# Kernel optimization log

Measured on AMD Instinct MI355X. Metric: run time of the kernel, lower is better.

Reference implementation:

```python
import jax, jax.numpy as jnp
import numpy as np
from jax import lax

# ---- fake-quant helpers (brevitas-style, STE round) ----

def ste_round(x):
    return x + lax.stop_gradient(jnp.round(x) - x)

def qsym(x, bits):
    """Symmetric per-tensor quant with dynamic max-abs scale."""
    qmax = float(2 ** (bits - 1) - 1)
    scale = jnp.max(jnp.abs(x)) / qmax + 1e-8
    return ste_round(jnp.clip(x / scale, -qmax - 1.0, qmax)) * scale

def qfixed(x, scale, lo, hi):
    """Fixed-scale quant (used for bounded activations sigmoid/tanh)."""
    return ste_round(jnp.clip(x / scale, lo, hi)) * scale

def qrelu(x, bits):
    """Unsigned quantized ReLU with dynamic per-tensor scale."""
    qmax = float(2 ** bits - 1)
    r = jax.nn.relu(x)
    scale = jnp.max(r) / qmax + 1e-8
    return ste_round(jnp.clip(r / scale, 0.0, qmax)) * scale

SIG_SCALE = 1.0 / 63.0    # 6-bit unsigned for sigmoid in [0,1]
TANH_SCALE = 1.0 / 31.0   # 6-bit signed for tanh in [-1,1]

IN, H = 10, 20


def setup_inputs() -> dict:
    key = jax.random.key(0)
    ks = jax.random.split(key, 12)
    s = lambda n: 1.0 / np.sqrt(n)
    return {
        "x": jax.random.normal(ks[0], (8192, 256, IN), jnp.float32),
        "w_ih": jax.random.uniform(ks[1], (4 * H, IN), jnp.float32, -s(H), s(H)),
        "w_hh": jax.random.uniform(ks[2], (4 * H, H), jnp.float32, -s(H), s(H)),
        "b_ih": jax.random.uniform(ks[3], (4 * H,), jnp.float32, -s(H), s(H)),
        "b_hh": jax.random.uniform(ks[4], (4 * H,), jnp.float32, -s(H), s(H)),
        "w1": jax.random.uniform(ks[5], (64, H), jnp.float32, -s(H), s(H)),
        "b1": jax.random.uniform(ks[6], (64,), jnp.float32, -s(H), s(H)),
        "w2": jax.random.uniform(ks[7], (32, 64), jnp.float32, -s(64), s(64)),
        "b2": jax.random.uniform(ks[8], (32,), jnp.float32, -s(64), s(64)),
        "w3": jax.random.uniform(ks[9], (5, 32), jnp.float32, -s(32), s(32)),
        "b3": jax.random.uniform(ks[10], (5,), jnp.float32, -s(32), s(32)),
    }


def reference(x, w_ih, w_hh, b_ih, b_hh, w1, b1, w2, b2, w3, b3):
    B, T, _ = x.shape
    # io quant (Int8 per-tensor) on input, 8-bit weight quant
    xq = qsym(x, 8)
    wih_q, whh_q = qsym(w_ih, 8), qsym(w_hh, 8)
    w1q, w2q, w3q = qsym(w1, 8), qsym(w2, 8), qsym(w3, 8)

    # precompute input contribution to gates: [B,T,4H]
    x_gates = jnp.einsum('bti,gi->btg', xq, wih_q) + b_ih + b_hh

    h0 = jnp.zeros((B, H), x.dtype)
    c0 = jnp.zeros((B, H), x.dtype)

    def step(carry, xg):
        h, c = carry
        gates = qsym(xg + h @ whh_q.T, 6)          # 6-bit gate accumulator
        i, f, g, o = jnp.split(gates, 4, axis=-1)   # torch gate order i,f,g,o
        i = qfixed(jax.nn.sigmoid(i), SIG_SCALE, 0.0, 63.0)
        f = qfixed(jax.nn.sigmoid(f), SIG_SCALE, 0.0, 63.0)
        g = qfixed(jnp.tanh(g), TANH_SCALE, -32.0, 31.0)
        o = qfixed(jax.nn.sigmoid(o), SIG_SCALE, 0.0, 63.0)
        c_new = qsym(f * c + i * g, 6)              # 6-bit cell state quant
        h_new = qsym(o * qfixed(jnp.tanh(c_new), TANH_SCALE, -32.0, 31.0), 8)  # io quant
        return (h_new, c_new), None

    (hT, _), _ = lax.scan(step, (h0, c0), jnp.swapaxes(x_gates, 0, 1))

    # dropout is identity in eval mode
    out = qrelu(hT, 6)
    out = qrelu(out @ w1q.T + b1, 6)
    out = qrelu(out @ w2q.T + b2, 6)
    return out @ w3q.T + b3
```

## Files before the change

### kernel.cpp

```cpp
#include <hip/hip_runtime.h>

constexpr int Tn  = 256;
constexpr int INn = 10;
constexpr int Hn  = 20;
constexpr int G4  = 80;
constexpr int Bn  = 8192;

constexpr int NB  = 256;
constexpr int NT  = 256;
constexpr int NW  = NT / 64;
constexpr int BPB = Bn / NB;
constexpr int PREP = 81;

constexpr int RING_U64  = 2 * NB;

constexpr int WS_XMAX   = 1040;
constexpr int WS_SX     = 1041;
constexpr int WS_WIH    = 1088;
constexpr int WS_WHH    = WS_WIH + G4 * INn;
constexpr int WS_W1     = WS_WHH + G4 * Hn;
constexpr int WS_W2     = WS_W1 + 64 * Hn;
constexpr int WS_W3     = WS_W2 + 32 * 64;
constexpr int WS_END    = WS_W3 + 5 * 32;

constexpr float SIGS = (float)(1.0 / 63.0);
constexpr float TANS = (float)(1.0 / 31.0);
constexpr double RS_SIG = 1.0 / (double)SIGS;
constexpr double RS_TAN = 1.0 / (double)TANS;

__device__ __forceinline__ float wave_bmax64(float v) {
#pragma unroll
  for (int off = 32; off; off >>= 1) v = fmaxf(v, __shfl_xor(v, off, 64));
  return v;
}

__device__ __forceinline__ float divrs(float v, double rs) {
  return (float)((double)v * rs);
}
__device__ __forceinline__ float quantq(float v, float s, float lo, float hi) {
  return __fmul_rn(rintf(fminf(fmaxf(v / s, lo), hi)), s);
}
__device__ __forceinline__ float quantr(float v, double rs, float s, float lo,
                                        float hi) {
  return __fmul_rn(rintf(fminf(fmaxf(divrs(v, rs), lo), hi)), s);
}
__device__ __forceinline__ float sigm(float v) {
  return 1.0f / (1.0f + expf(-v));
}

__device__ __forceinline__ unsigned long long ring_ld(unsigned long long* p) {
  return __hip_atomic_load(p, __ATOMIC_RELAXED, __HIP_MEMORY_SCOPE_AGENT);
}
__device__ __forceinline__ void ring_st(unsigned long long* p,
                                        unsigned long long v) {
  __hip_atomic_store(p, v, __ATOMIC_RELAXED, __HIP_MEMORY_SCOPE_AGENT);
}

__device__ __forceinline__ void gm_begin(float v, int inst,
                                         unsigned long long* ring,
                                         float* s_red) {
  const int tid = threadIdx.x;
  v = wave_bmax64(v);
  if ((tid & 63) == 0) s_red[tid >> 6] = v;
  __syncthreads();
  if (tid == 0) {
    float bm = fmaxf(fmaxf(s_red[0], s_red[1]), fmaxf(s_red[2], s_red[3]));
    ring_st(&ring[(inst & 1) * NB + blockIdx.x],
            ((unsigned long long)(unsigned)inst << 32) | __float_as_uint(bm));
  }
}

__device__ __forceinline__ float gm_end(int inst, unsigned long long* ring,
                                        float* s_bc) {
  const int tid = threadIdx.x;
  const unsigned long long tag = (unsigned long long)(unsigned)inst << 32;
  const int base = (inst & 1) * NB;
  if (tid < 64) {
    const int i0 = base + tid * 4;
    unsigned long long w0, w1, w2, w3;
    do {
      w0 = ring_ld(&ring[i0 + 0]);
      w1 = ring_ld(&ring[i0 + 1]);
      w2 = ring_ld(&ring[i0 + 2]);
      w3 = ring_ld(&ring[i0 + 3]);
    } while ((((w0 ^ tag) | (w1 ^ tag) | (w2 ^ tag) | (w3 ^ tag)) >> 32) != 0ull);
    float m = fmaxf(
        fmaxf(__uint_as_float((unsigned)w0), __uint_as_float((unsigned)w1)),
        fmaxf(__uint_as_float((unsigned)w2), __uint_as_float((unsigned)w3)));
    m = wave_bmax64(m);
    if (tid == 0) *s_bc = m;
  }
  __syncthreads();
  return *s_bc;
}

__global__ void k_init(unsigned long long* ring, unsigned* wsu) {
  int i = threadIdx.x;
  if (i < RING_U64) ring[i] = 0xFFFFFFFF00000000ull;
  if (i == 0) wsu[WS_XMAX] = 0u;
}

__global__ void k_xmax(const float4* __restrict__ x4, unsigned* wsu) {
  float m = 0.f;
  int idx = blockIdx.x * blockDim.x + threadIdx.x;
  int stride = gridDim.x * blockDim.x;
  for (int i = idx; i < (Bn * Tn * INn) / 4; i += stride) {
    float4 v = x4[i];
    m = fmaxf(m, fmaxf(fmaxf(fabsf(v.x), fabsf(v.y)),
                       fmaxf(fabsf(v.z), fabsf(v.w))));
  }
  m = wave_bmax64(m);
  __shared__ float sred[4];
  if ((threadIdx.x & 63) == 0) sred[threadIdx.x >> 6] = m;
  __syncthreads();
  if (threadIdx.x == 0) {
    m = fmaxf(fmaxf(sred[0], sred[1]), fmaxf(sred[2], sred[3]));
    atomicMax(&wsu[WS_XMAX], __float_as_uint(m));
  }
}

__device__ void quant_tensor(const float* __restrict__ src, int n, float* dst,
                             float* sred, float* sb, int nt) {
  const int tid = threadIdx.x;
  float m = 0.f;
  for (int i = tid; i < n; i += nt) m = fmaxf(m, fabsf(src[i]));
  m = wave_bmax64(m);
  __syncthreads();
  if ((tid & 63) == 0) sred[tid >> 6] = m;
  __syncthreads();
  if (tid == 0) {
    float bm = sred[0];
    for (int w = 1; w < nt / 64; ++w) bm = fmaxf(bm, sred[w]);
    *sb = __fadd_rn(bm / 127.0f, 1e-8f);
  }
  __syncthreads();
  float s = *sb;
  for (int i = tid; i < n; i += nt) {
    float q = rintf(fminf(fmaxf(src[i] / s, -128.f), 127.f));
    dst[i] = __fmul_rn(q, s);
  }
}

__global__ __launch_bounds__(1024) void k_wq(const float* wih, const float* whh,
                                             const float* w1, const float* w2,
                                             const float* w3, unsigned* wsu) {
  float* wsf = (float*)wsu;
  __shared__ float sred[16];
  __shared__ float sb;
  if (threadIdx.x == 0)
    wsf[WS_SX] = __fadd_rn(__uint_as_float(wsu[WS_XMAX]) / 127.0f, 1e-8f);
  quant_tensor(wih, G4 * INn, wsf + WS_WIH, sred, &sb, 1024);
  quant_tensor(whh, G4 * Hn,  wsf + WS_WHH, sred, &sb, 1024);
  quant_tensor(w1,  64 * Hn,  wsf + WS_W1,  sred, &sb, 1024);
  quant_tensor(w2,  32 * 64,  wsf + WS_W2,  sred, &sb, 1024);
  quant_tensor(w3,  5 * 32,   wsf + WS_W3,  sred, &sb, 1024);
}

__global__ __launch_bounds__(NT, 1) void k_lstm(
    const float* __restrict__ x,
    const float* __restrict__ bih, const float* __restrict__ bhh,
    const float* __restrict__ b1, const float* __restrict__ b2,
    const float* __restrict__ b3,
    float* __restrict__ out, unsigned* __restrict__ wsu) {
  const float* wsf = (const float*)wsu;
  unsigned long long* ring = (unsigned long long*)wsu;

  __shared__ float s_wih[G4][INn];
  __shared__ float s_whh[G4][Hn];
  __shared__ float s_bih[G4], s_bhh[G4];
  __shared__ float s_h[BPB][Hn];
  __shared__ float s_c[BPB][Hn];
  __shared__ float s_pre[BPB][PREP];
  __shared__ float s_xs[BPB][INn];
  __shared__ float s_l2[BPB][32];
  __shared__ float s_red[NW];
  __shared__ float s_bc;

  const int tid = threadIdx.x;
  const int b0 = blockIdx.x * BPB;

  for (int i = tid; i < G4 * INn; i += NT) (&s_wih[0][0])[i] = wsf[WS_WIH + i];
  for (int i = tid; i < G4 * Hn; i += NT) (&s_whh[0][0])[i] = wsf[WS_WHH + i];
  if (tid < G4) { s_bih[tid] = bih[tid]; s_bhh[tid] = bhh[tid]; }
  for (int i = tid; i < BPB * Hn; i += NT) {
    (&s_h[0][0])[i] = 0.f;
    (&s_c[0][0])[i] = 0.f;
  }
  const float sx = wsf[WS_SX];
  const double rsx = 1.0 / (double)sx;

  const int bl = tid >> 3;
  const int g0 = (tid & 7) * 10;

  const int bi0 = tid / INn, ii0 = tid - bi0 * INn;
  const int e1 = NT + tid;
  const int bi1 = e1 / INn, ii1 = e1 - bi1 * INn;
  const bool has1 = (e1 < BPB * INn);

  {
    float v = x[((b0 + bi0) * Tn + 0) * INn + ii0];
    s_xs[bi0][ii0] = __fmul_rn(rintf(fminf(fmaxf(divrs(v, rsx), -128.f), 127.f)), sx);
    if (has1) {
      float v1 = x[((b0 + bi1) * Tn + 0) * INn + ii1];
      s_xs[bi1][ii1] = __fmul_rn(rintf(fminf(fmaxf(divrs(v1, rsx), -128.f), 127.f)), sx);
    }
  }
  __syncthreads();

  float xacc[10];
  {
    float xr[INn];
#pragma unroll
    for (int i = 0; i < INn; i++) xr[i] = s_xs[bl][i];
#pragma unroll
    for (int gg = 0; gg < 10; ++gg) {
      int g = g0 + gg;
      float acc = 0.f;
#pragma unroll
      for (int i = 0; i < INn; i++) acc = fmaf(xr[i], s_wih[g][i], acc);
      acc = __fadd_rn(acc, s_bih[g]);
      xacc[gg] = __fadd_rn(acc, s_bhh[g]);
    }
  }

  int inst = 0;

  for (int t = 0; t < Tn; ++t) {
    const bool more = (t + 1 < Tn);

    float hreg[Hn];
#pragma unroll
    for (int k = 0; k < Hn; k++) hreg[k] = s_h[bl][k];
    float lm = 0.f;
#pragma unroll
    for (int gg = 0; gg < 10; ++gg) {
      int g = g0 + gg;
      float hd = 0.f;
#pragma unroll
      for (int k = 0; k < Hn; k++) hd = fmaf(hreg[k], s_whh[g][k], hd);
      float pre = __fadd_rn(xacc[gg], hd);
      s_pre[bl][g] = pre;
      lm = fmaxf(lm, fabsf(pre));
    }
    gm_begin(lm, inst, ring, s_red);
    float xr0 = 0.f, xr1 = 0.f;
    if (more) {
      xr0 = x[((b0 + bi0) * Tn + (t + 1)) * INn + ii0];
      if (has1) xr1 = x[((b0 + bi1) * Tn + (t + 1)) * INn + ii1];
    }
    float s1v = __fadd_rn(gm_end(inst, ring, &s_bc) / 31.0f, 1e-8f);
    inst++;
    const double rs1 = 1.0 / (double)s1v;

    float cpre[3], og[3], hpre[3];
    float lm2 = 0.f;
#pragma unroll
    for (int k = 0; k < 3; k++) {
      int e = tid + k * NT;
      if (e < BPB * Hn) {
        int cb = e / Hn, j = e - cb * Hn;
        float gi = quantr(s_pre[cb][j],      rs1, s1v, -32.f, 31.f);
        float gf = quantr(s_pre[cb][20 + j], rs1, s1v, -32.f, 31.f);
        float gg = quantr(s_pre[cb][40 + j], rs1, s1v, -32.f, 31.f);
        float go = quantr(s_pre[cb][60 + j], rs1, s1v, -32.f, 31.f);
        float iv = quantr(sigm(gi), RS_SIG, SIGS, 0.f, 63.f);
        float fv = quantr(sigm(gf), RS_SIG, SIGS, 0.f, 63.f);
        float gv = quantr(tanhf(gg), RS_TAN, TANS, -32.f, 31.f);
        og[k]    = quantr(sigm(go), RS_SIG, SIGS, 0.f, 63.f);
        float cp = __fadd_rn(__fmul_rn(fv, s_c[cb][j]), __fmul_rn(iv, gv));
        cpre[k] = cp;
        lm2 = fmaxf(lm2, fabsf(cp));
      }
    }
    gm_begin(lm2, inst, ring, s_red);
    if (more) {
      s_xs[bi0][ii0] = __fmul_rn(rintf(fminf(fmaxf(divrs(xr0, rsx), -128.f), 127.f)), sx);
      if (has1)
        s_xs[bi1][ii1] = __fmul_rn(rintf(fminf(fmaxf(divrs(xr1, rsx), -128.f), 127.f)), sx);
    }
    float s2v = __fadd_rn(gm_end(inst, ring, &s_bc) / 31.0f, 1e-8f);
    inst++;

    float lm3 = 0.f;
#pragma unroll
    for (int k = 0; k < 3; k++) {
      int e = tid + k * NT;
      if (e < BPB * Hn) {
        int cb = e / Hn, j = e - cb * Hn;
        float cn = quantq(cpre[k], s2v, -32.f, 31.f);
        s_c[cb][j] = cn;
        float tq = quantr(tanhf(cn), RS_TAN, TANS, -32.f, 31.f);
        float hp = __fmul_rn(og[k], tq);
        hpre[k] = hp;
        lm3 = fmaxf(lm3, fabsf(hp));
      }
    }
    gm_begin(lm3, inst, ring, s_red);
    if (more) {
      float xr[INn];
#pragma unroll
      for (int i = 0; i < INn; i++) xr[i] = s_xs[bl][i];
#pragma unroll
      for (int gg = 0; gg < 10; ++gg) {
        int g = g0 + gg;
        float acc = 0.f;
#pragma unroll
        for (int i = 0; i < INn; i++) acc = fmaf(xr[i], s_wih[g][i], acc);
        acc = __fadd_rn(acc, s_bih[g]);
        xacc[gg] = __fadd_rn(acc, s_bhh[g]);
      }
    }
    float s3v = __fadd_rn(gm_end(inst, ring, &s_bc) / 127.0f, 1e-8f);
    inst++;

#pragma unroll
    for (int k = 0; k < 3; k++) {
      int e = tid + k * NT;
      if (e < BPB * Hn) {
        int cb = e / Hn, j = e - cb * Hn;
        s_h[cb][j] = quantq(hpre[k], s3v, -128.f, 127.f);
      }
    }
    __syncthreads();
  }

  {
    float r[3];
    float lm = 0.f;
#pragma unroll
    for (int k = 0; k < 3; k++) {
      int e = tid + k * NT;
      if (e < BPB * Hn) {
        r[k] = fmaxf((&s_h[0][0])[e], 0.f);
        lm = fmaxf(lm, r[k]);
      }
    }
    gm_begin(lm, inst, ring, s_red);
    float s = __fadd_rn(gm_end(inst, ring, &s_bc) / 63.0f, 1e-8f);
    inst++;
#pragma unroll
    for (int k = 0; k < 3; k++) {
      int e = tid + k * NT;
      if (e < BPB * Hn)
        (&s_h[0][0])[e] = __fmul_rn(rintf(fminf(fmaxf(r[k] / s, 0.f), 63.f)), s);
    }
  }
  __syncthreads();

  float* s_l1 = &s_pre[0][0];
  {
    float a[8];
    float lm = 0.f;
#pragma unroll
    for (int k = 0; k < 8; k++) {
      int o = tid + k * NT;
      int cb = o >> 6, j = o & 63;
      float acc = 0.f;
#pragma unroll
      for (int kk = 0; kk < Hn; kk++)
        acc = fmaf(s_h[cb][kk], wsf[WS_W1 + j * Hn + kk], acc);
      acc = __fadd_rn(acc, b1[j]);
      acc = fmaxf(acc, 0.f);
      a[k] = acc;
      lm = fmaxf(lm, acc);
    }
    gm_begin(lm, inst, ring, s_red);
    float s = __fadd_rn(gm_end(inst, ring, &s_bc) / 63.0f, 1e-8f);
    inst++;
#pragma unroll
    for (int k = 0; k < 8; k++) {
      int o = tid + k * NT;
      s_l1[o] = __fmul_rn(rintf(fminf(fmaxf(a[k] / s, 0.f), 63.f)), s);
    }
  }
  __syncthreads();

  {
    float a[4];
    float lm = 0.f;
#pragma unroll
    for (int k = 0; k < 4; k++) {
      int o = tid + k * NT;
      int cb = o >> 5, j = o & 31;
      float acc = 0.f;
#pragma unroll
      for (int kk = 0; kk < 64; kk++)
        acc = fmaf(s_l1[cb * 64 + kk], wsf[WS_W2 + j * 64 + kk], acc);
      acc = __fadd_rn(acc, b2[j]);
      acc = fmaxf(acc, 0.f);
      a[k] = acc;
      lm = fmaxf(lm, acc);
    }
    gm_begin(lm, inst, ring, s_red);
    float s = __fadd_rn(gm_end(inst, ring, &s_bc) / 63.0f, 1e-8f);
    inst++;
#pragma unroll
    for (int k = 0; k < 4; k++) {
      int o = tid + k * NT;
      int cb = o >> 5, j = o & 31;
      s_l2[cb][j] = __fmul_rn(rintf(fminf(fmaxf(a[k] / s, 0.f), 63.f)), s);
    }
  }
  __syncthreads();

  if (tid < BPB * 5) {
    int cb = tid / 5, j = tid - cb * 5;
    float acc = 0.f;
#pragma unroll
    for (int kk = 0; kk < 32; kk++)
      acc = fmaf(s_l2[cb][kk], wsf[WS_W3 + j * 32 + kk], acc);
    acc = __fadd_rn(acc, b3[j]);
    out[(b0 + cb) * 5 + j] = acc;
  }
}

extern "C" void kernel_launch(void* const* d_in, const int* in_sizes, int n_in,
                              void* d_out, int out_size, void* d_ws,
                              size_t ws_size, hipStream_t stream) {
  const float* x   = (const float*)d_in[0];
  const float* wih = (const float*)d_in[1];
  const float* whh = (const float*)d_in[2];
  const float* bih = (const float*)d_in[3];
  const float* bhh = (const float*)d_in[4];
  const float* w1  = (const float*)d_in[5];
  const float* b1  = (const float*)d_in[6];
  const float* w2  = (const float*)d_in[7];
  const float* b2  = (const float*)d_in[8];
  const float* w3  = (const float*)d_in[9];
  const float* b3  = (const float*)d_in[10];
  float* out = (float*)d_out;
  unsigned* wsu = (unsigned*)d_ws;
  unsigned long long* ring = (unsigned long long*)d_ws;

  k_init<<<dim3(1), dim3(1024), 0, stream>>>(ring, wsu);
  k_xmax<<<dim3(512), dim3(256), 0, stream>>>((const float4*)x, wsu);
  k_wq<<<dim3(1), dim3(1024), 0, stream>>>(wih, whh, w1, w2, w3, wsu);

  void* args[] = {(void*)&x,  (void*)&bih, (void*)&bhh, (void*)&b1,
                  (void*)&b2, (void*)&b3,  (void*)&out, (void*)&wsu};
  hipLaunchCooperativeKernel(k_lstm, dim3(NB), dim3(NT), args, 0, stream);
}
```

Baseline: 2.048 ms.

## Use fewer, larger blocks to shrink the grid-wide max barrier ring

Cuts the persistent grid from 256 blocks of 256 threads to 64 blocks of 1024 threads. Each grid-wide max-reduction barrier then polls only 64 ring slots, one per lane, instead of four per lane. The block-level reduction now covers a variable number of waves through shuffles, and the spin loop is software-pipelined with two outstanding loads. Each block now holds more batch rows and uses fewer CUs, which risks lower occupancy and lower per-step throughput.

```diff
diff --git a/kernel.cpp b/kernel.cpp
--- a/kernel.cpp
+++ b/kernel.cpp
@@ -6,8 +6,8 @@
 constexpr int G4  = 80;
 constexpr int Bn  = 8192;
 
-constexpr int NB  = 256;
-constexpr int NT  = 256;
+constexpr int NB  = 64;
+constexpr int NT  = 1024;
 constexpr int NW  = NT / 64;
 constexpr int BPB = Bn / NB;
 constexpr int PREP = 81;
@@ -63,31 +63,31 @@
   v = wave_bmax64(v);
   if ((tid & 63) == 0) s_red[tid >> 6] = v;
   __syncthreads();
-  if (tid == 0) {
-    float bm = fmaxf(fmaxf(s_red[0], s_red[1]), fmaxf(s_red[2], s_red[3]));
-    ring_st(&ring[(inst & 1) * NB + blockIdx.x],
-            ((unsigned long long)(unsigned)inst << 32) | __float_as_uint(bm));
+  if (tid < 64) {
+    float bm = (tid < NW) ? s_red[tid] : 0.f;
+#pragma unroll
+    for (int off = 1; off < NW; off <<= 1) bm = fmaxf(bm, __shfl_xor(bm, off, 64));
+    if (tid == 0)
+      ring_st(&ring[(inst & 1) * NB + 0 + blockIdx.x],
+              ((unsigned long long)(unsigned)inst << 32) | __float_as_uint(bm));
   }
 }
 
 __device__ __forceinline__ float gm_end(int inst, unsigned long long* ring,
                                         float* s_bc) {
   const int tid = threadIdx.x;
-  const unsigned long long tag = (unsigned long long)(unsigned)inst << 32;
-  const int base = (inst & 1) * NB;
+  const unsigned ep = (unsigned)inst;
   if (tid < 64) {
-    const int i0 = base + tid * 4;
-    unsigned long long w0, w1, w2, w3;
-    do {
-      w0 = ring_ld(&ring[i0 + 0]);
-      w1 = ring_ld(&ring[i0 + 1]);
-      w2 = ring_ld(&ring[i0 + 2]);
-      w3 = ring_ld(&ring[i0 + 3]);
-    } while ((((w0 ^ tag) | (w1 ^ tag) | (w2 ^ tag) | (w3 ^ tag)) >> 32) != 0ull);
-    float m = fmaxf(
-        fmaxf(__uint_as_float((unsigned)w0), __uint_as_float((unsigned)w1)),
-        fmaxf(__uint_as_float((unsigned)w2), __uint_as_float((unsigned)w3)));
-    m = wave_bmax64(m);
+    unsigned long long* p = &ring[(inst & 1) * NB + tid];
+    unsigned long long cur = ring_ld(p);
+    for (;;) {
+      unsigned long long n1 = ring_ld(p);
+      if (__all((unsigned)(cur >> 32) == ep)) break;
+      unsigned long long n2 = ring_ld(p);
+      if (__all((unsigned)(n1 >> 32) == ep)) { cur = n1; break; }
+      cur = n2;
+    }
+    float m = wave_bmax64(__uint_as_float((unsigned)cur));
     if (tid == 0) *s_bc = m;
   }
   __syncthreads();
```

Result: slower. 3.338 ms (+63.0%).

## Halve grid to 128 blocks with 64 batch rows per block

Applied to the files above, without the earlier changes.

Reduces the persistent grid from 256 to 128 blocks, so each block handles 64 batch rows and each thread computes 20 gates instead of 10. The goal is to cut the cost of the cross-block max-reduction barriers (three per timestep), since each gm_end poll now reads fewer ring slots and fewer blocks must arrive. In exchange, per-block work per step doubles and only half the CUs are used, so the serial per-step compute gets longer.

```diff
diff --git a/kernel.cpp b/kernel.cpp
--- a/kernel.cpp
+++ b/kernel.cpp
@@ -6,10 +6,11 @@
 constexpr int G4  = 80;
 constexpr int Bn  = 8192;
 
-constexpr int NB  = 256;
+constexpr int NB  = 128;
 constexpr int NT  = 256;
 constexpr int NW  = NT / 64;
 constexpr int BPB = Bn / NB;
+constexpr int NGT = 20;
 constexpr int PREP = 81;
 
 constexpr int RING_U64  = 2 * NB;
@@ -76,17 +77,13 @@
   const unsigned long long tag = (unsigned long long)(unsigned)inst << 32;
   const int base = (inst & 1) * NB;
   if (tid < 64) {
-    const int i0 = base + tid * 4;
-    unsigned long long w0, w1, w2, w3;
+    const int i0 = base + tid * 2;
+    unsigned long long w0, w1;
     do {
       w0 = ring_ld(&ring[i0 + 0]);
       w1 = ring_ld(&ring[i0 + 1]);
-      w2 = ring_ld(&ring[i0 + 2]);
-      w3 = ring_ld(&ring[i0 + 3]);
-    } while ((((w0 ^ tag) | (w1 ^ tag) | (w2 ^ tag) | (w3 ^ tag)) >> 32) != 0ull);
-    float m = fmaxf(
-        fmaxf(__uint_as_float((unsigned)w0), __uint_as_float((unsigned)w1)),
-        fmaxf(__uint_as_float((unsigned)w2), __uint_as_float((unsigned)w3)));
+    } while ((((w0 ^ tag) | (w1 ^ tag)) >> 32) != 0ull);
+    float m = fmaxf(__uint_as_float((unsigned)w0), __uint_as_float((unsigned)w1));
     m = wave_bmax64(m);
     if (tid == 0) *s_bc = m;
   }
@@ -189,31 +186,35 @@
   const float sx = wsf[WS_SX];
   const double rsx = 1.0 / (double)sx;
 
-  const int bl = tid >> 3;
-  const int g0 = (tid & 7) * 10;
+  const int bl = tid >> 2;
+  const int g0 = (tid & 3) * NGT;
 
   const int bi0 = tid / INn, ii0 = tid - bi0 * INn;
   const int e1 = NT + tid;
   const int bi1 = e1 / INn, ii1 = e1 - bi1 * INn;
-  const bool has1 = (e1 < BPB * INn);
+  const int e2 = 2 * NT + tid;
+  const int bi2 = e2 / INn, ii2 = e2 - bi2 * INn;
+  const bool has2 = (e2 < BPB * INn);
 
   {
     float v = x[((b0 + bi0) * Tn + 0) * INn + ii0];
     s_xs[bi0][ii0] = __fmul_rn(rintf(fminf(fmaxf(divrs(v, rsx), -128.f), 127.f)), sx);
-    if (has1) {
-      float v1 = x[((b0 + bi1) * Tn + 0) * INn + ii1];
-      s_xs[bi1][ii1] = __fmul_rn(rintf(fminf(fmaxf(divrs(v1, rsx), -128.f), 127.f)), sx);
-    }
-  }
-  __syncthreads();
-
-  float xacc[10];
+    float v1 = x[((b0 + bi1) * Tn + 0) * INn + ii1];
+    s_xs[bi1][ii1] = __fmul_rn(rintf(fminf(fmaxf(divrs(v1, rsx), -128.f), 127.f)), sx);
+    if (has2) {
+      float v2 = x[((b0 + bi2) * Tn + 0) * INn + ii2];
+      s_xs[bi2][ii2] = __fmul_rn(rintf(fminf(fmaxf(divrs(v2, rsx), -128.f), 127.f)), sx);
+    }
+  }
+  __syncthreads();
+
+  float xacc[NGT];
   {
     float xr[INn];
 #pragma unroll
     for (int i = 0; i < INn; i++) xr[i] = s_xs[bl][i];
 #pragma unroll
-    for (int gg = 0; gg < 10; ++gg) {
+    for (int gg = 0; gg < NGT; ++gg) {
       int g = g0 + gg;
       float acc = 0.f;
 #pragma unroll
@@ -233,7 +234,7 @@
     for (int k = 0; k < Hn; k++) hreg[k] = s_h[bl][k];
     float lm = 0.f;
 #pragma unroll
-    for (int gg = 0; gg < 10; ++gg) {
+    for (int gg = 0; gg < NGT; ++gg) {
       int g = g0 + gg;
       float hd = 0.f;
 #pragma unroll
@@ -243,57 +244,56 @@
       lm = fmaxf(lm, fabsf(pre));
     }
     gm_begin(lm, inst, ring, s_red);
-    float xr0 = 0.f, xr1 = 0.f;
+    float xr0 = 0.f, xr1 = 0.f, xr2 = 0.f;
     if (more) {
       xr0 = x[((b0 + bi0) * Tn + (t + 1)) * INn + ii0];
-      if (has1) xr1 = x[((b0 + bi1) * Tn + (t + 1)) * INn + ii1];
+      xr1 = x[((b0 + bi1) * Tn + (t + 1)) * INn + ii1];
+      if (has2) xr2 = x[((b0 + bi2) * Tn + (t + 1)) * INn + ii2];
     }
     float s1v = __fadd_rn(gm_end(inst, ring, &s_bc) / 31.0f, 1e-8f);
     inst++;
     const double rs1 = 1.0 / (double)s1v;
 
-    float cpre[3], og[3], hpre[3];
+    float cpre[5], og[5];
     float lm2 = 0.f;
 #pragma unroll
-    for (int k = 0; k < 3; k++) {
+    for (int k = 0; k < 5; k++) {
       int e = tid + k * NT;
-      if (e < BPB * Hn) {
-        int cb = e / Hn, j = e - cb * Hn;
-        float gi = quantr(s_pre[cb][j],      rs1, s1v, -32.f, 31.f);
-        float gf = quantr(s_pre[cb][20 + j], rs1, s1v, -32.f, 31.f);
-        float gg = quantr(s_pre[cb][40 + j], rs1, s1v, -32.f, 31.f);
-        float go = quantr(s_pre[cb][60 + j], rs1, s1v, -32.f, 31.f);
-        float iv = quantr(sigm(gi), RS_SIG, SIGS, 0.f, 63.f);
-        float fv = quantr(sigm(gf), RS_SIG, SIGS, 0.f, 63.f);
-        float gv = quantr(tanhf(gg), RS_TAN, TANS, -32.f, 31.f);
-        og[k]    = quantr(sigm(go), RS_SIG, SIGS, 0.f, 63.f);
-        float cp = __fadd_rn(__fmul_rn(fv, s_c[cb][j]), __fmul_rn(iv, gv));
-        cpre[k] = cp;
-        lm2 = fmaxf(lm2, fabsf(cp));
-      }
+      int cb = e / Hn, j = e - cb * Hn;
+      float gi = quantr(s_pre[cb][j],      rs1, s1v, -32.f, 31.f);
+      float gf = quantr(s_pre[cb][20 + j], rs1, s1v, -32.f, 31.f);
+      float gg = quantr(s_pre[cb][40 + j], rs1, s1v, -32.f, 31.f);
+      float go = quantr(s_pre[cb][60 + j], rs1, s1v, -32.f, 31.f);
+      float iv = quantr(sigm(gi), RS_SIG, SIGS, 0.f, 63.f);
+      float fv = quantr(sigm(gf), RS_SIG, SIGS, 0.f, 63.f);
+      float gv = quantr(tanhf(gg), RS_TAN, TANS, -32.f, 31.f);
+      og[k]    = quantr(sigm(go), RS_SIG, SIGS, 0.f, 63.f);
+      float cp = __fadd_rn(__fmul_rn(fv, s_c[cb][j]), __fmul_rn(iv, gv));
+      cpre[k] = cp;
+      lm2 = fmaxf(lm2, fabsf(cp));
     }
     gm_begin(lm2, inst, ring, s_red);
     if (more) {
       s_xs[bi0][ii0] = __fmul_rn(rintf(fminf(fmaxf(divrs(xr0, rsx), -128.f), 127.f)), sx);
-      if (has1)
-        s_xs[bi1][ii1] = __fmul_rn(rintf(fminf(fmaxf(divrs(xr1, rsx), -128.f), 127.f)), sx);
+      s_xs[bi1][ii1] = __fmul_rn(rintf(fminf(fmaxf(divrs(xr1, rsx), -128.f), 127.f)), sx);
+      if (has2)
+        s_xs[bi2][ii2] = __fmul_rn(rintf(fminf(fmaxf(divrs(xr2, rsx), -128.f), 127.f)), sx);
     }
     float s2v = __fadd_rn(gm_end(inst, ring, &s_bc) / 31.0f, 1e-8f);
     inst++;
 
+    float hpre[5];
     float lm3 = 0.f;
 #pragma unroll
-    for (int k = 0; k < 3; k++) {
+    for (int k = 0; k < 5; k++) {
       int e = tid + k * NT;
-      if (e < BPB * Hn) {
-        int cb = e / Hn, j = e - cb * Hn;
-        float cn = quantq(cpre[k], s2v, -32.f, 31.f);
-        s_c[cb][j] = cn;
-        float tq = quantr(tanhf(cn), RS_TAN, TANS, -32.f, 31.f);
-        float hp = __fmul_rn(og[k], tq);
-        hpre[k] = hp;
-        lm3 = fmaxf(lm3, fabsf(hp));
-      }
+      int cb = e / Hn, j = e - cb * Hn;
+      float cn = quantq(cpre[k], s2v, -32.f, 31.f);
+      s_c[cb][j] = cn;
+      float tq = quantr(tanhf(cn), RS_TAN, TANS, -32.f, 31.f);
+      float hp = __fmul_rn(og[k], tq);
+      hpre[k] = hp;
+      lm3 = fmaxf(lm3, fabsf(hp));
     }
     gm_begin(lm3, inst, ring, s_red);
     if (more) {
@@ -301,7 +301,7 @@
 #pragma unroll
       for (int i = 0; i < INn; i++) xr[i] = s_xs[bl][i];
 #pragma unroll
-      for (int gg = 0; gg < 10; ++gg) {
+      for (int gg = 0; gg < NGT; ++gg) {
         int g = g0 + gg;
         float acc = 0.f;
 #pragma unroll
@@ -314,45 +314,40 @@
     inst++;
 
 #pragma unroll
-    for (int k = 0; k < 3; k++) {
+    for (int k = 0; k < 5; k++) {
       int e = tid + k * NT;
-      if (e < BPB * Hn) {
-        int cb = e / Hn, j = e - cb * Hn;
-        s_h[cb][j] = quantq(hpre[k], s3v, -128.f, 127.f);
-      }
+      int cb = e / Hn, j = e - cb * Hn;
+      s_h[cb][j] = quantq(hpre[k], s3v, -128.f, 127.f);
     }
     __syncthreads();
   }
 
   {
-    float r[3];
+    float r[5];
     float lm = 0.f;
 #pragma unroll
-    for (int k = 0; k < 3; k++) {
+    for (int k = 0; k < 5; k++) {
       int e = tid + k * NT;
-      if (e < BPB * Hn) {
-        r[k] = fmaxf((&s_h[0][0])[e], 0.f);
-        lm = fmaxf(lm, r[k]);
-      }
+      r[k] = fmaxf((&s_h[0][0])[e], 0.f);
+      lm = fmaxf(lm, r[k]);
     }
     gm_begin(lm, inst, ring, s_red);
     float s = __fadd_rn(gm_end(inst, ring, &s_bc) / 63.0f, 1e-8f);
     inst++;
 #pragma unroll
-    for (int k = 0; k < 3; k++) {
+    for (int k = 0; k < 5; k++) {
       int e = tid + k * NT;
-      if (e < BPB * Hn)
-        (&s_h[0][0])[e] = __fmul_rn(rintf(fminf(fmaxf(r[k] / s, 0.f), 63.f)), s);
+      (&s_h[0][0])[e] = __fmul_rn(rintf(fminf(fmaxf(r[k] / s, 0.f), 63.f)), s);
     }
   }
   __syncthreads();
 
   float* s_l1 = &s_pre[0][0];
   {
-    float a[8];
+    float a[16];
     float lm = 0.f;
 #pragma unroll
-    for (int k = 0; k < 8; k++) {
+    for (int k = 0; k < 16; k++) {
       int o = tid + k * NT;
       int cb = o >> 6, j = o & 63;
       float acc = 0.f;
@@ -368,7 +363,7 @@
     float s = __fadd_rn(gm_end(inst, ring, &s_bc) / 63.0f, 1e-8f);
     inst++;
 #pragma unroll
-    for (int k = 0; k < 8; k++) {
+    for (int k = 0; k < 16; k++) {
       int o = tid + k * NT;
       s_l1[o] = __fmul_rn(rintf(fminf(fmaxf(a[k] / s, 0.f), 63.f)), s);
     }
@@ -376,10 +371,10 @@
   __syncthreads();
 
   {
-    float a[4];
+    float a[8];
     float lm = 0.f;
 #pragma unroll
-    for (int k = 0; k < 4; k++) {
+    for (int k = 0; k < 8; k++) {
       int o = tid + k * NT;
       int cb = o >> 5, j = o & 31;
       float acc = 0.f;
@@ -395,7 +390,7 @@
     float s = __fadd_rn(gm_end(inst, ring, &s_bc) / 63.0f, 1e-8f);
     inst++;
 #pragma unroll
-    for (int k = 0; k < 4; k++) {
+    for (int k = 0; k < 8; k++) {
       int o = tid + k * NT;
       int cb = o >> 5, j = o & 31;
       s_l2[cb][j] = __fmul_rn(rintf(fminf(fmaxf(a[k] / s, 0.f), 63.f)), s);
@@ -403,8 +398,8 @@
   }
   __syncthreads();
 
-  if (tid < BPB * 5) {
-    int cb = tid / 5, j = tid - cb * 5;
+  for (int o = tid; o < BPB * 5; o += NT) {
+    int cb = o / 5, j = o - cb * 5;
     float acc = 0.f;
 #pragma unroll
     for (int kk = 0; kk < 32; kk++)
```

Measured after the change: 2.516 ms. 1.23x slower.
